# Optimization experiments

Hardware: AMD Instinct MI355X
Metric: run time of the kernel (lower is better)

The kernel has to match this reference:

```python
import jax, jax.numpy as jnp
import numpy as np

B, S, D = 2, 2048, 2048
H, KVH = 32, 8
HD = D // H            # 64
G = H // KVH           # 4 kv groups
SCALE = 1.0 / np.sqrt(HD)


def setup_inputs() -> dict:
    key = jax.random.key(0)
    k1, k2, k3, k4, k5 = jax.random.split(key, 5)
    hidden_states = jax.random.normal(k1, (B, S, D), dtype=jnp.float32)
    Wq = jax.random.normal(k2, (D, H * HD), dtype=jnp.float32) * 0.02
    Wk = jax.random.normal(k3, (D, KVH * HD), dtype=jnp.float32) * 0.02
    Wv = jax.random.normal(k4, (D, KVH * HD), dtype=jnp.float32) * 0.02
    Wo = jax.random.normal(k5, (H * HD, D), dtype=jnp.float32) * 0.02
    return {"hidden_states": hidden_states, "Wq": Wq, "Wk": Wk, "Wv": Wv, "Wo": Wo}


def reference(hidden_states, Wq, Wk, Wv, Wo):
    B_, S_, _ = hidden_states.shape
    q = (hidden_states @ Wq).reshape(B_, S_, H, HD).transpose(0, 2, 1, 3)      # [B,H,S,HD]
    k = (hidden_states @ Wk).reshape(B_, S_, KVH, HD).transpose(0, 2, 1, 3)    # [B,KVH,S,HD]
    v = (hidden_states @ Wv).reshape(B_, S_, KVH, HD).transpose(0, 2, 1, 3)
    # repeat_interleave over head dim: kv head g serves q heads [g*G, (g+1)*G)
    k = jnp.repeat(k, G, axis=1)  # [B,H,S,HD]
    v = jnp.repeat(v, G, axis=1)
    scores = jnp.einsum('bhqd,bhkd->bhqk', q, k) * SCALE
    probs = jax.nn.softmax(scores.astype(jnp.float32), axis=-1).astype(q.dtype)
    # dropout is identity in eval mode
    out = jnp.einsum('bhqk,bhkd->bhqd', probs, v)             # [B,H,S,HD]
    out = out.transpose(0, 2, 1, 3).reshape(B_, S_, H * HD)   # [B,S,D]
    return out @ Wo
```

## Files before the change

kernel.cpp:

```cpp
#include <hip/hip_runtime.h>
#include <hip/hip_bf16.h>

typedef unsigned short u16;
typedef __attribute__((ext_vector_type(8))) short short8;
typedef __attribute__((ext_vector_type(4))) float f32x4;
typedef __attribute__((ext_vector_type(16))) float f32x16;
typedef __attribute__((ext_vector_type(4))) unsigned short u16x4;
typedef __attribute__((ext_vector_type(4))) int int4v;

#define S_LEN 2048
#define NH 32
#define NKV 8
#define QSCALE 0.18033688011112042f
#define PSHIFT 14.0f

__device__ __forceinline__ float fexp2(float x) { return __builtin_amdgcn_exp2f(x); }

__device__ __forceinline__ u16 f2bf(float f) {
  unsigned int u = __builtin_bit_cast(unsigned int, f);
  u += 0x7fffu + ((u >> 16) & 1u);
  return (u16)(u >> 16);
}

__device__ __forceinline__ unsigned int pk2bf(float a, float b) {
  float2 t; t.x = a; t.y = b;
  __hip_bfloat162 h = __float22bfloat162_rn(t);
  unsigned int r;
  __builtin_memcpy(&r, &h, 4);
  return r;
}

__device__ __forceinline__ void async16(const void* g, void* l) {
  __builtin_amdgcn_global_load_lds(
      (__attribute__((address_space(1))) void*)g,
      (__attribute__((address_space(3))) void*)l, 16, 0, 0);
}

__device__ __forceinline__ short8 mk_pf(unsigned a, unsigned b, unsigned c, unsigned d) {
  int4v t; t.x = (int)a; t.y = (int)b; t.z = (int)c; t.w = (int)d;
  return __builtin_bit_cast(short8, t);
}

__global__ __launch_bounds__(256) void prep_kernel(const float* __restrict__ X,
                                                   const float* __restrict__ Wq,
                                                   const float* __restrict__ Wk,
                                                   const float* __restrict__ Wv,
                                                   const float* __restrict__ Wo,
                                                   u16* __restrict__ Xb,
                                                   u16* __restrict__ Wqt,
                                                   u16* __restrict__ Wkt,
                                                   u16* __restrict__ Wvt,
                                                   u16* __restrict__ Wot) {
  __shared__ float tile[32][33];
  int bx = blockIdx.x, tid = threadIdx.x;
  if (bx < 8192) {
    int idx = bx * 256 + tid;
    float4 v = ((const float4*)X)[idx];
    u16x4 o;
    o.x = f2bf(v.x); o.y = f2bf(v.y); o.z = f2bf(v.z); o.w = f2bf(v.w);
    *(u16x4*)&Xb[(size_t)idx * 4] = o;
    return;
  }
  const float* in; u16* out; int N, bi;
  if (bx < 12288)      { bi = bx - 8192;  in = Wq; out = Wqt; N = 2048; }
  else if (bx < 13312) { bi = bx - 12288; in = Wk; out = Wkt; N = 512; }
  else if (bx < 14336) { bi = bx - 13312; in = Wv; out = Wvt; N = 512; }
  else                 { bi = bx - 14336; in = Wo; out = Wot; N = 2048; }
  const int K = 2048;
  int nbx = N >> 5;
  int n0 = (bi % nbx) * 32, k0 = (bi / nbx) * 32;
  int tx = tid & 31, ty = tid >> 5;
#pragma unroll
  for (int i = 0; i < 32; i += 8)
    tile[ty + i][tx] = in[(size_t)(k0 + ty + i) * N + n0 + tx];
  __syncthreads();
#pragma unroll
  for (int i = 0; i < 32; i += 8)
    out[(size_t)(n0 + ty + i) * K + k0 + tx] = f2bf(tile[tx][ty + i]);
}

__global__ __launch_bounds__(256) void gemm_qkv(const u16* __restrict__ A,
                                                const u16* __restrict__ Wqt,
                                                const u16* __restrict__ Wkvt,
                                                u16* __restrict__ Qb,
                                                u16* __restrict__ KVb) {
  __shared__ u16 la0[4096], la1[4096], lb0[4096], lb1[4096];
  int tid = threadIdx.x, bx = blockIdx.x;
  int mode, bm, bn;
  const u16* Bt;
  if (bx < 512) {
    mode = 0; Bt = Wqt;
    int x = bx & 7, i = bx >> 3;
    bm = (x >> 1) * 8 + (i >> 3);
    bn = (x & 1) * 8 + (i & 7);
  } else {
    mode = 1; Bt = Wkvt;
    int b2 = bx - 512;
    int x = b2 & 7, i = b2 >> 3;
    bm = (x >> 1) * 8 + (i >> 2);
    bn = (x & 1) * 4 + (i & 3);
  }
  const int K = 2048;
  int w = tid >> 6, lane = tid & 63, qd = lane >> 4, ln = lane & 15;
  int wm = w >> 1, wn = w & 1;
  f32x4 acc[4][4];
#pragma unroll
  for (int i = 0; i < 4; ++i)
#pragma unroll
    for (int j = 0; j < 4; ++j) acc[i][j] = {0.f, 0.f, 0.f, 0.f};

  const u16* Ab = A + (size_t)bm * 128 * K;
  const u16* Bb = Bt + (size_t)bn * 128 * K;
  int row0 = tid >> 2, c0 = tid & 3;
  int g0 = c0 ^ (row0 & 3) ^ ((row0 >> 2) & 3);
  int s1 = tid + 256, row1 = s1 >> 2, c1 = s1 & 3;
  int g1 = c1 ^ (row1 & 3) ^ ((row1 >> 2) & 3);
  int pat = (ln & 3) ^ ((ln >> 2) & 3);
  int goff = (qd ^ pat) * 8;
  const u16* pa0 = Ab + (size_t)row0 * K + g0 * 8;
  const u16* pa1 = Ab + (size_t)row1 * K + g1 * 8;
  const u16* pb0 = Bb + (size_t)row0 * K + g0 * 8;
  const u16* pb1 = Bb + (size_t)row1 * K + g1 * 8;

#define QKV_STAGE(LA, LB, OFS)                      \
  async16(pa0 + (OFS), &LA[tid * 8]);               \
  async16(pa1 + (OFS), &LA[2048 + tid * 8]);        \
  async16(pb0 + (OFS), &LB[tid * 8]);               \
  async16(pb1 + (OFS), &LB[2048 + tid * 8]);

#define QKV_COMPUTE(LA, LB)                                                        \
  {                                                                                \
    short8 af[4], bf[4];                                                           \
    _Pragma("unroll") for (int i = 0; i < 4; ++i)                                  \
        af[i] = *(const short8*)&LA[(wm * 64 + i * 16 + ln) * 32 + goff];          \
    _Pragma("unroll") for (int j = 0; j < 4; ++j)                                  \
        bf[j] = *(const short8*)&LB[(wn * 64 + j * 16 + ln) * 32 + goff];          \
    __builtin_amdgcn_s_setprio(1);                                                 \
    _Pragma("unroll") for (int i = 0; i < 4; ++i)                                  \
      _Pragma("unroll") for (int j = 0; j < 4; ++j)                                \
        acc[i][j] =                                                                \
            __builtin_amdgcn_mfma_f32_16x16x32_bf16(af[i], bf[j], acc[i][j], 0, 0, 0); \
    __builtin_amdgcn_s_setprio(0);                                                 \
  }

  QKV_STAGE(la0, lb0, 0);
  __syncthreads();

  for (int kt = 0; kt < K; kt += 64) {
    QKV_STAGE(la1, lb1, kt + 32);
    QKV_COMPUTE(la0, lb0);
    __syncthreads();
    if (kt + 64 < K) { QKV_STAGE(la0, lb0, kt + 64); }
    QKV_COMPUTE(la1, lb1);
    __syncthreads();
  }
#undef QKV_STAGE
#undef QKV_COMPUTE

#pragma unroll
  for (int i = 0; i < 4; ++i)
#pragma unroll
    for (int r = 0; r < 4; ++r) {
      int m = bm * 128 + wm * 64 + i * 16 + qd * 4 + r;
      int b = m >> 11, s = m & 2047;
#pragma unroll
      for (int j = 0; j < 4; ++j) {
        int n = bn * 128 + wn * 64 + j * 16 + ln;
        float v = acc[i][j][r];
        int hh = n >> 6, hd = n & 63;
        if (mode == 0) {
          Qb[(((size_t)(b * NH + hh)) * S_LEN + s) * 64 + hd] = f2bf(v * QSCALE);
        } else {
          if (hh < 8)
            KVb[(((size_t)(b * NKV + hh)) * S_LEN + s) * 64 + hd] = f2bf(v);
          else
            KVb[2097152 + (((size_t)(b * NKV + (hh - 8))) * 64 + hd) * S_LEN + s] = f2bf(v);
        }
      }
    }
}

__global__ __launch_bounds__(256) void gemm_out(const u16* __restrict__ A,
                                                const u16* __restrict__ Bt,
                                                float* __restrict__ outp) {
  __shared__ u16 la0[4096], la1[4096], lb0[4096], lb1[4096];
  const int K = 2048, N = 2048;
  int tid = threadIdx.x;
  int x = blockIdx.x & 7, ii = blockIdx.x >> 3;
  int bm = (x >> 1) * 8 + (ii >> 3);
  int bn = (x & 1) * 8 + (ii & 7);
  int w = tid >> 6, lane = tid & 63, qd = lane >> 4, ln = lane & 15;
  int wm = w >> 1, wn = w & 1;
  f32x4 acc[4][4];
#pragma unroll
  for (int i = 0; i < 4; ++i)
#pragma unroll
    for (int j = 0; j < 4; ++j) acc[i][j] = {0.f, 0.f, 0.f, 0.f};

  const u16* Ab = A + (size_t)bm * 128 * K;
  const u16* Bb = Bt + (size_t)bn * 128 * K;
  int row0 = tid >> 2, c0 = tid & 3;
  int g0 = c0 ^ (row0 & 3) ^ ((row0 >> 2) & 3);
  int s1 = tid + 256, row1 = s1 >> 2, c1 = s1 & 3;
  int g1 = c1 ^ (row1 & 3) ^ ((row1 >> 2) & 3);
  int pat = (ln & 3) ^ ((ln >> 2) & 3);
  int goff = (qd ^ pat) * 8;
  const u16* pa0 = Ab + (size_t)row0 * K + g0 * 8;
  const u16* pa1 = Ab + (size_t)row1 * K + g1 * 8;
  const u16* pb0 = Bb + (size_t)row0 * K + g0 * 8;
  const u16* pb1 = Bb + (size_t)row1 * K + g1 * 8;

#define OUT_STAGE(LA, LB, OFS)                      \
  async16(pa0 + (OFS), &LA[tid * 8]);               \
  async16(pa1 + (OFS), &LA[2048 + tid * 8]);        \
  async16(pb0 + (OFS), &LB[tid * 8]);               \
  async16(pb1 + (OFS), &LB[2048 + tid * 8]);

#define OUT_COMPUTE(LA, LB)                                                        \
  {                                                                                \
    short8 af[4], bf[4];                                                           \
    _Pragma("unroll") for (int i = 0; i < 4; ++i)                                  \
        af[i] = *(const short8*)&LA[(wm * 64 + i * 16 + ln) * 32 + goff];          \
    _Pragma("unroll") for (int j = 0; j < 4; ++j)                                  \
        bf[j] = *(const short8*)&LB[(wn * 64 + j * 16 + ln) * 32 + goff];          \
    __builtin_amdgcn_s_setprio(1);                                                 \
    _Pragma("unroll") for (int i = 0; i < 4; ++i)                                  \
      _Pragma("unroll") for (int j = 0; j < 4; ++j)                                \
        acc[i][j] =                                                                \
            __builtin_amdgcn_mfma_f32_16x16x32_bf16(af[i], bf[j], acc[i][j], 0, 0, 0); \
    __builtin_amdgcn_s_setprio(0);                                                 \
  }

  OUT_STAGE(la0, lb0, 0);
  __syncthreads();

  for (int kt = 0; kt < K; kt += 64) {
    OUT_STAGE(la1, lb1, kt + 32);
    OUT_COMPUTE(la0, lb0);
    __syncthreads();
    if (kt + 64 < K) { OUT_STAGE(la0, lb0, kt + 64); }
    OUT_COMPUTE(la1, lb1);
    __syncthreads();
  }
#undef OUT_STAGE
#undef OUT_COMPUTE

#pragma unroll
  for (int i = 0; i < 4; ++i)
#pragma unroll
    for (int r = 0; r < 4; ++r) {
      int m = bm * 128 + wm * 64 + i * 16 + qd * 4 + r;
#pragma unroll
      for (int j = 0; j < 4; ++j) {
        int n = bn * 128 + wn * 64 + j * 16 + ln;
        outp[(size_t)m * N + n] = acc[i][j][r];
      }
    }
}

__global__ __launch_bounds__(256, 2) void attn_kernel(const u16* __restrict__ Q,
                                                      const u16* __restrict__ K,
                                                      const u16* __restrict__ VT,
                                                      u16* __restrict__ Ao) {
  __shared__ u16 sh[16384];
  int tid = threadIdx.x;
  int w = tid >> 6, lane = tid & 63;
  int l31 = lane & 31, l5 = lane >> 5;
  int qt = blockIdx.x >> 6, bh = blockIdx.x & 63;
  int b = bh >> 5, h = bh & 31, g = h >> 2;
  const u16* gQ = Q + ((size_t)bh * S_LEN + qt * 256) * 64;
  const u16* gK = K + (size_t)(b * NKV + g) * S_LEN * 64;
  const u16* gV = VT + (size_t)(b * NKV + g) * 64 * S_LEN;

  int p7 = l31 & 7;

  int s0 = tid, r0 = s0 >> 3, c0 = s0 & 7, gg0 = c0 ^ (r0 & 7);
  int s1 = tid + 256, r1 = s1 >> 3, c1 = s1 & 7, gg1 = c1 ^ (r1 & 7);

#pragma unroll
  for (int k = 0; k < 8; ++k) {
    int s = tid + k * 256;
    int q = s >> 3, c = s & 7, gg = c ^ (q & 7);
    async16(gQ + (size_t)q * 64 + gg * 8, &sh[s * 8]);
  }
  __syncthreads();
  short8 qf[2][4];
#pragma unroll
  for (int qg = 0; qg < 2; ++qg) {
    int qrow = w * 64 + qg * 32 + l31;
#pragma unroll
    for (int ks = 0; ks < 4; ++ks)
      qf[qg][ks] = *(const short8*)&sh[qrow * 64 + ((ks * 2 + l5) ^ p7) * 8];
  }
  __syncthreads();

  async16(gK + (size_t)r0 * 64 + gg0 * 8, &sh[s0 * 8]);
  async16(gK + (size_t)r1 * 64 + gg1 * 8, &sh[s1 * 8]);
  async16(gV + (size_t)r0 * S_LEN + gg0 * 8, &sh[8192 + s0 * 8]);
  async16(gV + (size_t)r1 * S_LEN + gg1 * 8, &sh[8192 + s1 * 8]);
  __syncthreads();

  const f32x16 psh16 = {-PSHIFT, -PSHIFT, -PSHIFT, -PSHIFT, -PSHIFT, -PSHIFT,
                        -PSHIFT, -PSHIFT, -PSHIFT, -PSHIFT, -PSHIFT, -PSHIFT,
                        -PSHIFT, -PSHIFT, -PSHIFT, -PSHIFT};
  f32x16 accA0, accA1, accB0, accB1;
#pragma unroll
  for (int t = 0; t < 16; ++t) { accA0[t] = 0.f; accA1[t] = 0.f; accB0[t] = 0.f; accB1[t] = 0.f; }
  float liA = 0.f, liB = 0.f;

#define SOFTMAX32(SC, LI, PF0, PF1)                                              \
  short8 PF0, PF1;                                                               \
  {                                                                              \
    float p[16];                                                                 \
    _Pragma("unroll") for (int t = 0; t < 16; ++t) p[t] = fexp2(SC[t]);          \
    _Pragma("unroll") for (int t = 0; t < 16; t += 4)                            \
        LI += (p[t] + p[t + 1]) + (p[t + 2] + p[t + 3]);                         \
    unsigned W[8];                                                               \
    _Pragma("unroll") for (int t = 0; t < 8; ++t) W[t] = pk2bf(p[2 * t], p[2 * t + 1]); \
    auto ra = __builtin_amdgcn_permlane32_swap((int)W[0], (int)W[2], false, false); \
    auto rb = __builtin_amdgcn_permlane32_swap((int)W[1], (int)W[3], false, false); \
    auto rc = __builtin_amdgcn_permlane32_swap((int)W[4], (int)W[6], false, false); \
    auto rd = __builtin_amdgcn_permlane32_swap((int)W[5], (int)W[7], false, false); \
    PF0 = mk_pf((unsigned)ra[0], (unsigned)rb[0], (unsigned)ra[1], (unsigned)rb[1]); \
    PF1 = mk_pf((unsigned)rc[0], (unsigned)rd[0], (unsigned)rc[1], (unsigned)rd[1]); \
  }

  for (int c = 0; c < 32; ++c) {
    int cur = c & 1;
    if (c < 31) {
      int nb = cur ^ 1, cn = c + 1;
      async16(gK + (size_t)(cn * 64 + r0) * 64 + gg0 * 8, &sh[nb * 4096 + s0 * 8]);
      async16(gK + (size_t)(cn * 64 + r1) * 64 + gg1 * 8, &sh[nb * 4096 + s1 * 8]);
      async16(gV + (size_t)r0 * S_LEN + cn * 64 + gg0 * 8, &sh[8192 + nb * 4096 + s0 * 8]);
      async16(gV + (size_t)r1 * S_LEN + cn * 64 + gg1 * 8, &sh[8192 + nb * 4096 + s1 * 8]);
    }
    const u16* kb = &sh[cur * 4096];
    const u16* vb = &sh[8192 + cur * 4096];

#pragma unroll
    for (int kblk = 0; kblk < 2; ++kblk) {
      f32x16 scA = psh16, scB = psh16;
      __builtin_amdgcn_s_setprio(1);
#pragma unroll
      for (int ks = 0; ks < 4; ++ks) {
        short8 kf = *(const short8*)&kb[(kblk * 32 + l31) * 64 + ((ks * 2 + l5) ^ p7) * 8];
        scA = __builtin_amdgcn_mfma_f32_32x32x16_bf16(kf, qf[0][ks], scA, 0, 0, 0);
        scB = __builtin_amdgcn_mfma_f32_32x32x16_bf16(kf, qf[1][ks], scB, 0, 0, 0);
      }
      __builtin_amdgcn_s_setprio(0);

      SOFTMAX32(scA, liA, pfA0, pfA1)
      SOFTMAX32(scB, liB, pfB0, pfB1)

      __builtin_amdgcn_s_setprio(1);
#pragma unroll
      for (int hb = 0; hb < 2; ++hb) {
        short8 vf = *(const short8*)&vb[(hb * 32 + l31) * 64 + ((kblk * 4 + l5) ^ p7) * 8];
        if (hb == 0) {
          accA0 = __builtin_amdgcn_mfma_f32_32x32x16_bf16(vf, pfA0, accA0, 0, 0, 0);
          accB0 = __builtin_amdgcn_mfma_f32_32x32x16_bf16(vf, pfB0, accB0, 0, 0, 0);
        } else {
          accA1 = __builtin_amdgcn_mfma_f32_32x32x16_bf16(vf, pfA0, accA1, 0, 0, 0);
          accB1 = __builtin_amdgcn_mfma_f32_32x32x16_bf16(vf, pfB0, accB1, 0, 0, 0);
        }
      }
#pragma unroll
      for (int hb = 0; hb < 2; ++hb) {
        short8 vf = *(const short8*)&vb[(hb * 32 + l31) * 64 + ((kblk * 4 + 2 + l5) ^ p7) * 8];
        if (hb == 0) {
          accA0 = __builtin_amdgcn_mfma_f32_32x32x16_bf16(vf, pfA1, accA0, 0, 0, 0);
          accB0 = __builtin_amdgcn_mfma_f32_32x32x16_bf16(vf, pfB1, accB0, 0, 0, 0);
        } else {
          accA1 = __builtin_amdgcn_mfma_f32_32x32x16_bf16(vf, pfA1, accA1, 0, 0, 0);
          accB1 = __builtin_amdgcn_mfma_f32_32x32x16_bf16(vf, pfB1, accB1, 0, 0, 0);
        }
      }
      __builtin_amdgcn_s_setprio(0);
    }
    __syncthreads();
  }
#undef SOFTMAX32

  {
    float l = liA + __shfl_xor(liA, 32);
    float inv = 1.f / l;
    int q = qt * 256 + w * 64 + l31;
    size_t base = ((size_t)b * S_LEN + q) * 2048 + h * 64;
#pragma unroll
    for (int rq = 0; rq < 4; ++rq) {
      u16x4 o0, o1;
#pragma unroll
      for (int rr = 0; rr < 4; ++rr) {
        o0[rr] = f2bf(accA0[rq * 4 + rr] * inv);
        o1[rr] = f2bf(accA1[rq * 4 + rr] * inv);
      }
      *(u16x4*)&Ao[base + rq * 8 + l5 * 4] = o0;
      *(u16x4*)&Ao[base + 32 + rq * 8 + l5 * 4] = o1;
    }
  }
  {
    float l = liB + __shfl_xor(liB, 32);
    float inv = 1.f / l;
    int q = qt * 256 + w * 64 + 32 + l31;
    size_t base = ((size_t)b * S_LEN + q) * 2048 + h * 64;
#pragma unroll
    for (int rq = 0; rq < 4; ++rq) {
      u16x4 o0, o1;
#pragma unroll
      for (int rr = 0; rr < 4; ++rr) {
        o0[rr] = f2bf(accB0[rq * 4 + rr] * inv);
        o1[rr] = f2bf(accB1[rq * 4 + rr] * inv);
      }
      *(u16x4*)&Ao[base + rq * 8 + l5 * 4] = o0;
      *(u16x4*)&Ao[base + 32 + rq * 8 + l5 * 4] = o1;
    }
  }
}

extern "C" void kernel_launch(void* const* d_in, const int* in_sizes, int n_in,
                              void* d_out, int out_size, void* d_ws, size_t ws_size,
                              hipStream_t stream) {
  const float* X  = (const float*)d_in[0];
  const float* Wq = (const float*)d_in[1];
  const float* Wk = (const float*)d_in[2];
  const float* Wv = (const float*)d_in[3];
  const float* Wo = (const float*)d_in[4];
  char* ws = (char*)d_ws;
  u16* Xb  = (u16*)(ws);
  u16* Wqt = (u16*)(ws + 16777216);
  u16* Wkt = (u16*)(ws + 25165824);
  u16* Wvt = (u16*)(ws + 27262976);
  u16* Wot = (u16*)(ws + 29360128);
  u16* Qb  = (u16*)(ws + 37748736);
  u16* Kb  = (u16*)(ws + 54525952);
  u16* VTb = (u16*)(ws + 58720256);
  u16* Ab  = (u16*)(ws + 62914560);
  float* out = (float*)d_out;

  prep_kernel<<<18432, 256, 0, stream>>>(X, Wq, Wk, Wv, Wo, Xb, Wqt, Wkt, Wvt, Wot);
  gemm_qkv<<<768, 256, 0, stream>>>(Xb, Wqt, Wkt, Qb, Kb);
  attn_kernel<<<512, 256, 0, stream>>>(Qb, Kb, VTb, Ab);
  gemm_out<<<512, 256, 0, stream>>>(Ab, Wot, out);
}
```

Before: 302.6 us.

## Compute softmax row sums with MFMA against ones and vectorize V stores

The attention kernel no longer sums exp values with VALU adds. It accumulates row sums through extra MFMA instructions that multiply a bf16 ones operand by the packed probability fragments. This moves work from VALU to the matrix unit, adds four MFMAs per kblk plus two extra f32x16 accumulators, and sums the bf16-rounded probabilities, which can slightly change numerics. Separately, the QKV epilogue now writes the transposed V output as packed 4-element vector stores instead of scattered scalar stores.

```diff
diff --git a/kernel.cpp b/kernel.cpp
--- a/kernel.cpp
+++ b/kernel.cpp
@@ -158,26 +158,31 @@
 #undef QKV_COMPUTE
 
 #pragma unroll
-  for (int i = 0; i < 4; ++i)
-#pragma unroll
-    for (int r = 0; r < 4; ++r) {
-      int m = bm * 128 + wm * 64 + i * 16 + qd * 4 + r;
-      int b = m >> 11, s = m & 2047;
-#pragma unroll
-      for (int j = 0; j < 4; ++j) {
-        int n = bn * 128 + wn * 64 + j * 16 + ln;
-        float v = acc[i][j][r];
-        int hh = n >> 6, hd = n & 63;
-        if (mode == 0) {
-          Qb[(((size_t)(b * NH + hh)) * S_LEN + s) * 64 + hd] = f2bf(v * QSCALE);
-        } else {
-          if (hh < 8)
-            KVb[(((size_t)(b * NKV + hh)) * S_LEN + s) * 64 + hd] = f2bf(v);
-          else
-            KVb[2097152 + (((size_t)(b * NKV + (hh - 8))) * 64 + hd) * S_LEN + s] = f2bf(v);
-        }
-      }
-    }
+  for (int i = 0; i < 4; ++i) {
+    int m0 = bm * 128 + wm * 64 + i * 16 + qd * 4;
+    int b = m0 >> 11, s0 = m0 & 2047;
+#pragma unroll
+    for (int j = 0; j < 4; ++j) {
+      int n = bn * 128 + wn * 64 + j * 16 + ln;
+      int hh = n >> 6, hd = n & 63;
+      if (mode == 0) {
+#pragma unroll
+        for (int r = 0; r < 4; ++r)
+          Qb[(((size_t)(b * NH + hh)) * S_LEN + s0 + r) * 64 + hd] =
+              f2bf(acc[i][j][r] * QSCALE);
+      } else if (hh < 8) {
+#pragma unroll
+        for (int r = 0; r < 4; ++r)
+          KVb[(((size_t)(b * NKV + hh)) * S_LEN + s0 + r) * 64 + hd] =
+              f2bf(acc[i][j][r]);
+      } else {
+        u16x4 o;
+#pragma unroll
+        for (int r = 0; r < 4; ++r) o[r] = f2bf(acc[i][j][r]);
+        *(u16x4*)&KVb[2097152 + (((size_t)(b * NKV + (hh - 8))) * 64 + hd) * S_LEN + s0] = o;
+      }
+    }
+  }
 }
 
 __global__ __launch_bounds__(256) void gemm_out(const u16* __restrict__ A,
@@ -304,17 +309,21 @@
                         -PSHIFT, -PSHIFT, -PSHIFT, -PSHIFT, -PSHIFT, -PSHIFT,
                         -PSHIFT, -PSHIFT, -PSHIFT, -PSHIFT};
   f32x16 accA0, accA1, accB0, accB1;
-#pragma unroll
-  for (int t = 0; t < 16; ++t) { accA0[t] = 0.f; accA1[t] = 0.f; accB0[t] = 0.f; accB1[t] = 0.f; }
-  float liA = 0.f, liB = 0.f;
-
-#define SOFTMAX32(SC, LI, PF0, PF1)                                              \
+  f32x16 laccA, laccB;
+#pragma unroll
+  for (int t = 0; t < 16; ++t) {
+    accA0[t] = 0.f; accA1[t] = 0.f; accB0[t] = 0.f; accB1[t] = 0.f;
+    laccA[t] = 0.f; laccB[t] = 0.f;
+  }
+  short8 ones8;
+#pragma unroll
+  for (int t = 0; t < 8; ++t) ones8[t] = (short)0x3F80;
+
+#define SOFTMAX32(SC, PF0, PF1)                                                  \
   short8 PF0, PF1;                                                               \
   {                                                                              \
     float p[16];                                                                 \
     _Pragma("unroll") for (int t = 0; t < 16; ++t) p[t] = fexp2(SC[t]);          \
-    _Pragma("unroll") for (int t = 0; t < 16; t += 4)                            \
-        LI += (p[t] + p[t + 1]) + (p[t + 2] + p[t + 3]);                         \
     unsigned W[8];                                                               \
     _Pragma("unroll") for (int t = 0; t < 8; ++t) W[t] = pk2bf(p[2 * t], p[2 * t + 1]); \
     auto ra = __builtin_amdgcn_permlane32_swap((int)W[0], (int)W[2], false, false); \
@@ -349,10 +358,12 @@
       }
       __builtin_amdgcn_s_setprio(0);
 
-      SOFTMAX32(scA, liA, pfA0, pfA1)
-      SOFTMAX32(scB, liB, pfB0, pfB1)
+      SOFTMAX32(scA, pfA0, pfA1)
+      SOFTMAX32(scB, pfB0, pfB1)
 
       __builtin_amdgcn_s_setprio(1);
+      laccA = __builtin_amdgcn_mfma_f32_32x32x16_bf16(ones8, pfA0, laccA, 0, 0, 0);
+      laccB = __builtin_amdgcn_mfma_f32_32x32x16_bf16(ones8, pfB0, laccB, 0, 0, 0);
 #pragma unroll
       for (int hb = 0; hb < 2; ++hb) {
         short8 vf = *(const short8*)&vb[(hb * 32 + l31) * 64 + ((kblk * 4 + l5) ^ p7) * 8];
@@ -364,6 +375,8 @@
           accB1 = __builtin_amdgcn_mfma_f32_32x32x16_bf16(vf, pfB0, accB1, 0, 0, 0);
         }
       }
+      laccA = __builtin_amdgcn_mfma_f32_32x32x16_bf16(ones8, pfA1, laccA, 0, 0, 0);
+      laccB = __builtin_amdgcn_mfma_f32_32x32x16_bf16(ones8, pfB1, laccB, 0, 0, 0);
 #pragma unroll
       for (int hb = 0; hb < 2; ++hb) {
         short8 vf = *(const short8*)&vb[(hb * 32 + l31) * 64 + ((kblk * 4 + 2 + l5) ^ p7) * 8];
@@ -382,8 +395,7 @@
 #undef SOFTMAX32
 
   {
-    float l = liA + __shfl_xor(liA, 32);
-    float inv = 1.f / l;
+    float inv = 1.f / laccA[0];
     int q = qt * 256 + w * 64 + l31;
     size_t base = ((size_t)b * S_LEN + q) * 2048 + h * 64;
 #pragma unroll
@@ -399,8 +411,7 @@
     }
   }
   {
-    float l = liB + __shfl_xor(liB, 32);
-    float inv = 1.f / l;
+    float inv = 1.f / laccB[0];
     int q = qt * 256 + w * 64 + 32 + l31;
     size_t base = ((size_t)b * S_LEN + q) * 2048 + h * 64;
 #pragma unroll
```

Measured after the change: 302.4 us. No clear change (-0.1%).
